# Performance work log

Hardware: AMD Instinct MI355X
Metric: run time of the kernel (lower is better)

## Reference

```python
import jax, jax.numpy as jnp
import numpy as np

B, SQ, SKV, D = 4, 2048, 2048, 2048
NEG = -1e9


def setup_inputs() -> dict:
    key = jax.random.key(0)
    ks = jax.random.split(key, 7)
    x = jax.random.normal(ks[0], (B, SKV, D), dtype=jnp.float32)
    enc_q = jax.random.normal(ks[1], (B, SQ, D), dtype=jnp.float32)
    enc_k = jax.random.normal(ks[2], (B, SKV, D), dtype=jnp.float32)
    i_mask = jax.random.bernoulli(ks[3], 0.1, (B, SQ, SKV))  # True -> masked
    s = 1.0 / np.sqrt(D)
    Wq = jax.random.normal(ks[4], (D, D), dtype=jnp.float32) * s
    Wk = jax.random.normal(ks[5], (D, D), dtype=jnp.float32) * s
    Wv = jax.random.normal(ks[6], (D, D), dtype=jnp.float32) * s
    return {"x": x, "enc_q": enc_q, "enc_k": enc_k, "i_mask": i_mask,
            "Wq": Wq, "Wk": Wk, "Wv": Wv}


def reference(x, enc_q, enc_k, i_mask, Wq, Wk, Wv):
    # Bias-free linear projections (nn.Linear: y = x @ W^T)
    q = jnp.einsum('bsd,ed->bse', enc_q, Wq)   # [B,SQ,D]
    k = jnp.einsum('bsd,ed->bse', enc_k, Wk)   # [B,SKV,D]
    v = jnp.einsum('bsd,ed->bse', x, Wv)       # [B,SKV,D]
    scale = 1.0 / jnp.sqrt(jnp.asarray(q.shape[-1], q.dtype))
    scores = jnp.einsum('bqd,bkd->bqk', q, k) * scale  # [B,SQ,SKV]
    scores = jnp.where(i_mask, jnp.asarray(NEG, scores.dtype), scores)
    attn = jax.nn.softmax(scores, axis=-1)
    return jnp.einsum('bqk,bkd->bqd', attn, v)  # [B,SQ,D]
```

## Files before the change

### kernel.cpp

```cpp
#include <hip/hip_runtime.h>
#include <stdint.h>

typedef short  short8  __attribute__((ext_vector_type(8)));
typedef unsigned short ushort8 __attribute__((ext_vector_type(8)));
typedef float  f32x4   __attribute__((ext_vector_type(4)));

#define BB  4
#define SQL 2048
#define SKL 2048
#define NEGV -1e9f
#define AS1 __attribute__((address_space(1)))
#define AS3 __attribute__((address_space(3)))

__device__ __forceinline__ unsigned short f2bf(float f){
  union { float f; uint32_t u; } x; x.f = f;
  return (unsigned short)((x.u + 0x7FFFu + ((x.u >> 16) & 1u)) >> 16);
}
__device__ __forceinline__ float bf2f(unsigned short h){
  union { uint32_t u; float f; } x; x.u = ((uint32_t)h) << 16;
  return x.f;
}

#define BARR() __builtin_amdgcn_s_barrier()
#define LGKM0() { asm volatile("s_waitcnt lgkmcnt(0)" ::: "memory"); __builtin_amdgcn_sched_barrier(0); }
#define VM0()   { asm volatile("s_waitcnt vmcnt(0)"   ::: "memory"); __builtin_amdgcn_sched_barrier(0); }

__global__ void mask_detect(const uint8_t* __restrict__ m, int* __restrict__ cnt){
  const long n4 = (long)BB * SQL * SKL / 4;
  long idx  = (long)blockIdx.x * blockDim.x + threadIdx.x;
  long step = (long)gridDim.x * blockDim.x;
  int c0 = 0, c1 = 0, c2 = 0;
  for (long i4 = idx; i4 < n4; i4 += step){
    uchar4 b = ((const uchar4*)m)[i4];
    c0 += (b.y != 0) + (b.z != 0) + (b.w != 0);
    c1 += (b.x > 1) + (b.y > 1) + (b.z > 1) + (b.w > 1);
    c2 += (b.y != 0);
  }
  #pragma unroll
  for (int o = 32; o >= 1; o >>= 1){
    c0 += __shfl_xor(c0, o); c1 += __shfl_xor(c1, o); c2 += __shfl_xor(c2, o);
  }
  if ((threadIdx.x & 63) == 0){
    atomicAdd(&cnt[0], c0); atomicAdd(&cnt[1], c1); atomicAdd(&cnt[2], c2);
  }
}

__global__ __launch_bounds__(256)
void cvt6(const float* __restrict__ s0, const float* __restrict__ s1,
          const float* __restrict__ s2, const float* __restrict__ s3,
          const float* __restrict__ s4, const float* __restrict__ s5,
          unsigned short* __restrict__ d0, unsigned short* __restrict__ d1,
          unsigned short* __restrict__ d2, unsigned short* __restrict__ d3,
          unsigned short* __restrict__ d4, unsigned short* __restrict__ d5)
{
  const long total = 7864320;
  for (long c = (long)blockIdx.x * blockDim.x + threadIdx.x; c < total;
       c += (long)gridDim.x * blockDim.x){
    const float* s; unsigned short* d; long off;
    if      (c < 2097152){ s = s0; d = d0; off = c; }
    else if (c < 4194304){ s = s1; d = d1; off = c - 2097152; }
    else if (c < 6291456){ s = s2; d = d2; off = c - 4194304; }
    else if (c < 6815744){ s = s3; d = d3; off = c - 6291456; }
    else if (c < 7340032){ s = s4; d = d4; off = c - 6815744; }
    else                 { s = s5; d = d5; off = c - 7340032; }
    f32x4 a = ((const f32x4*)s)[off * 2];
    f32x4 b = ((const f32x4*)s)[off * 2 + 1];
    ushort8 w;
    #pragma unroll
    for (int j = 0; j < 4; ++j){ w[j] = f2bf(a[j]); w[j + 4] = f2bf(b[j]); }
    ((ushort8*)d)[off] = w;
  }
}

template<int EPI>
__device__ __forceinline__ void gemm256_body(
    const unsigned short* __restrict__ Ag, const unsigned short* __restrict__ Bg,
    void* __restrict__ Cb, const void* __restrict__ mask, const int* __restrict__ cnt,
    int bz, long Cbs, long tm, long tn, float scale,
    unsigned short (&lA)[2][16384], unsigned short (&lB)[2][16384])
{
  constexpr int LD = 2048;
  const int tid = threadIdx.x, lane = tid & 63, wid = tid >> 6;
  const int wm = wid >> 2, wn = wid & 3;
  const int l15 = lane & 15, l16 = lane >> 4;

  f32x4 acc[8][4] = {};

  auto stage = [&](unsigned short* dst, const unsigned short* src, long tbase, int k){
    #pragma unroll
    for (int l = 0; l < 4; ++l){
      const int idx = l * 512 + tid;
      const int row = idx >> 3;
      const int gsw = (idx & 7) ^ (row & 7);
      __builtin_amdgcn_global_load_lds(
        (const AS1 void*)(src + (tbase + row) * LD + k + gsw * 8),
        (AS3 void*)(dst + idx * 8), 16, 0, 0);
    }
  };

  short8 aF[4], bF[4];
  #define RDA(BUF, MH, KS)                                                    \
    _Pragma("unroll")                                                         \
    for (int j = 0; j < 4; ++j){                                              \
      const int fr = wm * 128 + ((MH) * 4 + j) * 16 + l15;                    \
      const int g  = (KS) * 4 + l16;                                          \
      aF[j] = *(const short8*)&lA[BUF][(fr * 8 + (g ^ (fr & 7))) * 8];        \
    }
  #define RDB(BUF, KS)                                                        \
    _Pragma("unroll")                                                         \
    for (int j = 0; j < 4; ++j){                                              \
      const int fn = wn * 64 + j * 16 + l15;                                  \
      const int g  = (KS) * 4 + l16;                                          \
      bF[j] = *(const short8*)&lB[BUF][(fn * 8 + (g ^ (fn & 7))) * 8];        \
    }
  #define MFMA16(MH)                                                          \
    _Pragma("unroll")                                                         \
    for (int j = 0; j < 4; ++j){                                              \
      _Pragma("unroll")                                                       \
      for (int n = 0; n < 4; ++n)                                             \
        acc[(MH) * 4 + j][n] = __builtin_amdgcn_mfma_f32_16x16x32_bf16(       \
            aF[j], bF[n], acc[(MH) * 4 + j][n], 0, 0, 0);                     \
    }

  #define KTILE(BUF, KST, DOSTAGE)                                            \
  {                                                                           \
                                             \
    RDB(BUF, 0); RDA(BUF, 0, 0);                                              \
    if (DOSTAGE) stage(lA[(BUF) ^ 1], Ag, tm, (KST));                         \
    BARR(); LGKM0();                                                          \
    __builtin_amdgcn_s_setprio(1); MFMA16(0); __builtin_amdgcn_s_setprio(0);  \
    BARR();                                                                   \
                                             \
    RDA(BUF, 1, 0);                                                           \
    if (DOSTAGE) stage(lB[(BUF) ^ 1], Bg, tn, (KST));                         \
    BARR(); LGKM0();                                                          \
    __builtin_amdgcn_s_setprio(1); MFMA16(1); __builtin_amdgcn_s_setprio(0);  \
    BARR();                                                                   \
                                                            \
    RDB(BUF, 1); RDA(BUF, 0, 1);                                              \
    BARR(); LGKM0();                                                          \
    __builtin_amdgcn_s_setprio(1); MFMA16(0); __builtin_amdgcn_s_setprio(0);  \
    BARR();                                                                   \
         \
    RDA(BUF, 1, 1);                                                           \
    BARR(); LGKM0();                                                          \
    __builtin_amdgcn_s_setprio(1); MFMA16(1); __builtin_amdgcn_s_setprio(0);  \
    VM0();                                                                    \
    BARR();                                                                   \
  }

  stage(lA[0], Ag, tm, 0);
  stage(lB[0], Bg, tn, 0);
  VM0(); BARR();

  for (int it = 0; it < 16; ++it){
    KTILE(0, (2 * it + 1) * 64, true);
    KTILE(1, (2 * it + 2) * 64, it < 15);
  }

  const int colo = l15, rowg = l16 * 4;
  if constexpr (EPI == 0){
    unsigned short* C = (unsigned short*)Cb + (long)bz * Cbs;
    #pragma unroll
    for (int m = 0; m < 8; ++m)
      #pragma unroll
      for (int j = 0; j < 4; ++j){
        const long row = tm + wm * 128 + m * 16 + rowg + j;
        unsigned short* cr = C + row * LD + tn + wn * 64 + colo;
        #pragma unroll
        for (int n = 0; n < 4; ++n) cr[n * 16] = f2bf(acc[m][n][j]);
      }
  } else if constexpr (EPI == 2){
    float* C = (float*)Cb + (long)bz * Cbs;
    #pragma unroll
    for (int m = 0; m < 8; ++m)
      #pragma unroll
      for (int j = 0; j < 4; ++j){
        const long row = tm + wm * 128 + m * 16 + rowg + j;
        float* cr = C + row * LD + tn + wn * 64 + colo;
        #pragma unroll
        for (int n = 0; n < 4; ++n) cr[n * 16] = acc[m][n][j];
      }
  } else {
    const int a0 = cnt[0], a1 = cnt[1], a2 = cnt[2];
    const int mmode = (a1 == 0) ? (a0 > 1000 ? 0 : 1) : (a2 > 1000 ? 2 : 3);
    unsigned short* C = (unsigned short*)Cb + (long)bz * Cbs;
    const long mbase = (long)bz * SQL * SKL;
    #pragma unroll
    for (int m = 0; m < 8; ++m)
      #pragma unroll
      for (int j = 0; j < 4; ++j){
        const long row = tm + wm * 128 + m * 16 + rowg + j;
        #pragma unroll
        for (int n = 0; n < 4; ++n){
          const long col = tn + wn * 64 + n * 16 + colo;
          const long midx = mbase + row * SKL + col;
          bool msk;
          if (mmode == 0)      msk = ((const uint8_t*)mask)[midx] != 0;
          else if (mmode == 1) msk = ((const int*)mask)[midx] != 0;
          else if (mmode == 2) msk = ((const unsigned short*)mask)[midx] != 0;
          else                 msk = ((const uint32_t*)mask)[midx] != 0;
          float vv = acc[m][n][j] * scale;
          if (msk) vv = NEGV;
          C[row * SKL + col] = f2bf(vv);
        }
      }
  }
  #undef RDA
  #undef RDB
  #undef MFMA16
  #undef KTILE
}

__device__ __forceinline__ void xcd_decode(int& bx, int& by, int& bz){
  const int gx = gridDim.x, gy = gridDim.y;
  const int nwg = gx * gy * gridDim.z;
  const int lid = blockIdx.x + gx * (blockIdx.y + gy * blockIdx.z);
  const int sw  = (lid & 7) * (nwg >> 3) + (lid >> 3);
  bx = sw % gx;
  const int t = sw / gx;
  by = t % gy;
  bz = t / gy;
}

template<int EPI>
__global__ __launch_bounds__(512, 2)
void gemm256(const unsigned short* __restrict__ A, const unsigned short* __restrict__ B,
             void* __restrict__ Cb, const void* __restrict__ mask,
             const int* __restrict__ cnt, long Abs, long Bbs, long Cbs, float scale)
{
  __shared__ unsigned short lA[2][16384];
  __shared__ unsigned short lB[2][16384];
  int bx, by, bz; xcd_decode(bx, by, bz);
  gemm256_body<EPI>(A + (long)bz * Abs, B + (long)bz * Bbs, Cb, mask, cnt, bz, Cbs,
                    (long)by * 256, (long)bx * 256, scale, lA, lB);
}

__global__ __launch_bounds__(512, 2)
void gemm256_proj3(const unsigned short* A0, const unsigned short* A1, const unsigned short* A2,
                   const unsigned short* B0, const unsigned short* B1, const unsigned short* B2,
                   void* C0, void* C1, void* C2)
{
  __shared__ unsigned short lA[2][16384];
  __shared__ unsigned short lB[2][16384];
  int bx, by, bz; xcd_decode(bx, by, bz);
  const int sec = bz >> 2, b = bz & 3;
  const long NN = (long)SQL * 2048;
  const unsigned short* Av = sec == 0 ? A0 : sec == 1 ? A1 : A2;
  const unsigned short* Bv = sec == 0 ? B0 : sec == 1 ? B1 : B2;
  void*                 Cv = sec == 0 ? C0 : sec == 1 ? C1 : C2;
  const long Abs = (sec == 2) ? 0 : NN;
  const long Bbs = (sec == 2) ? NN : 0;
  gemm256_body<0>(Av + (long)b * Abs, Bv + (long)b * Bbs, Cv, nullptr, nullptr, b, NN,
                  (long)by * 256, (long)bx * 256, 1.f, lA, lB);
}

template<int AMODE, int BMODE, int EPI>
__device__ __forceinline__ void gemm_body(
    const void* __restrict__ Av, const void* __restrict__ Bv,
    void* __restrict__ Cb, const void* __restrict__ mask, const int* __restrict__ cnt,
    int bz, long Abs, long Bbs, long Cbs, long tm, long tn, float scale,
    unsigned short (*lA)[4096], unsigned short (*lB)[4096])
{
  constexpr int K = 2048, LD = 2048;
  const int tid = threadIdx.x, lane = tid & 63, wave = tid >> 6;
  const int wr = wave >> 1, wc = wave & 1;
  const int c0 = tid, c1 = tid + 256;
  const int r0 = c0 >> 2, q0 = (c0 & 3) * 8;
  const int r1 = c1 >> 2, q1 = (c1 & 3) * 8;

  const unsigned short* A16 = (const unsigned short*)Av + (long)bz * Abs;
  const unsigned short* B16 = (const unsigned short*)Bv + (long)bz * Bbs;
  const float*          A32 = (const float*)Av + (long)bz * Abs;
  const float*          B32 = (const float*)Bv + (long)bz * Bbs;

  f32x4 acc[4][4] = {};
  f32x4 sA[4], sB[4];

  auto issueA = [&](int buf, int kk){
    if constexpr (AMODE == 0){
      __builtin_amdgcn_global_load_lds((const AS1 void*)(A16 + (tm + r0) * LD + q0 + kk),
                                       (AS3 void*)(lA[buf] + c0 * 8), 16, 0, 0);
      __builtin_amdgcn_global_load_lds((const AS1 void*)(A16 + (tm + r1) * LD + q1 + kk),
                                       (AS3 void*)(lA[buf] + c1 * 8), 16, 0, 0);
    } else {
      sA[0] = *(const f32x4*)(A32 + (tm + r0) * LD + q0 + kk);
      sA[1] = *(const f32x4*)(A32 + (tm + r0) * LD + q0 + kk + 4);
      sA[2] = *(const f32x4*)(A32 + (tm + r1) * LD + q1 + kk);
      sA[3] = *(const f32x4*)(A32 + (tm + r1) * LD + q1 + kk + 4);
    }
  };
  auto issueB = [&](int buf, int kk){
    if constexpr (BMODE == 0){
      __builtin_amdgcn_global_load_lds((const AS1 void*)(B16 + (tn + r0) * LD + q0 + kk),
                                       (AS3 void*)(lB[buf] + c0 * 8), 16, 0, 0);
      __builtin_amdgcn_global_load_lds((const AS1 void*)(B16 + (tn + r1) * LD + q1 + kk),
                                       (AS3 void*)(lB[buf] + c1 * 8), 16, 0, 0);
    } else {
      sB[0] = *(const f32x4*)(B32 + (tn + r0) * LD + q0 + kk);
      sB[1] = *(const f32x4*)(B32 + (tn + r0) * LD + q0 + kk + 4);
      sB[2] = *(const f32x4*)(B32 + (tn + r1) * LD + q1 + kk);
      sB[3] = *(const f32x4*)(B32 + (tn + r1) * LD + q1 + kk + 4);
    }
  };
  auto writeA = [&](int buf){
    if constexpr (AMODE == 1){
      ushort8 w0, w1;
      #pragma unroll
      for (int j = 0; j < 4; ++j){
        w0[j] = f2bf(sA[0][j]); w0[j + 4] = f2bf(sA[1][j]);
        w1[j] = f2bf(sA[2][j]); w1[j + 4] = f2bf(sA[3][j]);
      }
      *(ushort8*)(lA[buf] + c0 * 8) = w0;
      *(ushort8*)(lA[buf] + c1 * 8) = w1;
    }
  };
  auto writeB = [&](int buf){
    if constexpr (BMODE == 1){
      ushort8 w0, w1;
      #pragma unroll
      for (int j = 0; j < 4; ++j){
        w0[j] = f2bf(sB[0][j]); w0[j + 4] = f2bf(sB[1][j]);
        w1[j] = f2bf(sB[2][j]); w1[j + 4] = f2bf(sB[3][j]);
      }
      *(ushort8*)(lB[buf] + c0 * 8) = w0;
      *(ushort8*)(lB[buf] + c1 * 8) = w1;
    }
  };
  auto computeTile = [&](int buf){
    short8 aF[4], bF[4];
    #pragma unroll
    for (int m = 0; m < 4; ++m)
      aF[m] = *(const short8*)(lA[buf] + (wr * 64 + m * 16 + (lane & 15)) * 32 + (lane >> 4) * 8);
    #pragma unroll
    for (int n = 0; n < 4; ++n)
      bF[n] = *(const short8*)(lB[buf] + (wc * 64 + n * 16 + (lane & 15)) * 32 + (lane >> 4) * 8);
    #pragma unroll
    for (int m = 0; m < 4; ++m)
      #pragma unroll
      for (int n = 0; n < 4; ++n)
        acc[m][n] = __builtin_amdgcn_mfma_f32_16x16x32_bf16(aF[m], bF[n], acc[m][n], 0, 0, 0);
  };

  issueA(0, 0); issueB(0, 0); writeA(0); writeB(0);
  __syncthreads();
  int cur = 0;
  for (int k0 = 0; k0 < K - 32; k0 += 32){
    issueA(cur ^ 1, k0 + 32);
    issueB(cur ^ 1, k0 + 32);
    computeTile(cur);
    writeA(cur ^ 1); writeB(cur ^ 1);
    __syncthreads();
    cur ^= 1;
  }
  computeTile(cur);

  const int colo = lane & 15, rowg = (lane >> 4) * 4;
  if constexpr (EPI == 0){
    unsigned short* C = (unsigned short*)Cb + (long)bz * Cbs;
    #pragma unroll
    for (int m = 0; m < 4; ++m)
      #pragma unroll
      for (int j = 0; j < 4; ++j){
        const long row = tm + wr * 64 + m * 16 + rowg + j;
        unsigned short* cr = C + row * LD + tn + wc * 64 + colo;
        #pragma unroll
        for (int n = 0; n < 4; ++n) cr[n * 16] = f2bf(acc[m][n][j]);
      }
  } else if constexpr (EPI == 2){
    float* C = (float*)Cb + (long)bz * Cbs;
    #pragma unroll
    for (int m = 0; m < 4; ++m)
      #pragma unroll
      for (int j = 0; j < 4; ++j){
        const long row = tm + wr * 64 + m * 16 + rowg + j;
        float* cr = C + row * LD + tn + wc * 64 + colo;
        #pragma unroll
        for (int n = 0; n < 4; ++n) cr[n * 16] = acc[m][n][j];
      }
  } else {
    const int a0 = cnt[0], a1 = cnt[1], a2 = cnt[2];
    const int mmode = (a1 == 0) ? (a0 > 1000 ? 0 : 1) : (a2 > 1000 ? 2 : 3);
    unsigned short* C = (unsigned short*)Cb + (long)bz * Cbs;
    const long mbase = (long)bz * SQL * SKL;
    #pragma unroll
    for (int m = 0; m < 4; ++m)
      #pragma unroll
      for (int j = 0; j < 4; ++j){
        const long row = tm + wr * 64 + m * 16 + rowg + j;
        #pragma unroll
        for (int n = 0; n < 4; ++n){
          const long col = tn + wc * 64 + n * 16 + colo;
          const long midx = mbase + row * SKL + col;
          bool msk;
          if (mmode == 0)      msk = ((const uint8_t*)mask)[midx] != 0;
          else if (mmode == 1) msk = ((const int*)mask)[midx] != 0;
          else if (mmode == 2) msk = ((const unsigned short*)mask)[midx] != 0;
          else                 msk = ((const uint32_t*)mask)[midx] != 0;
          float vv = acc[m][n][j] * scale;
          if (msk) vv = NEGV;
          C[row * SKL + col] = f2bf(vv);
        }
      }
  }
}

template<int AMODE, int BMODE, int EPI>
__global__ __launch_bounds__(256, 2)
void gemm_nt(const void* __restrict__ Abv, const void* __restrict__ Bbv,
             void* __restrict__ Cb, const void* __restrict__ mask,
             const int* __restrict__ cnt,
             long Abs, long Bbs, long Cbs, float scale)
{
  __shared__ unsigned short lA[2][4096];
  __shared__ unsigned short lB[2][4096];
  int bx, by, bz; xcd_decode(bx, by, bz);
  gemm_body<AMODE, BMODE, EPI>(Abv, Bbv, Cb, mask, cnt, bz, Abs, Bbs, Cbs,
                               (long)by * 128, (long)bx * 128, scale, lA, lB);
}

template<int MODE>
__global__ __launch_bounds__(256, 2)
void gemm_proj3(const void* A0, const void* A1, const void* A2,
                const void* B0, const void* B1, const void* B2,
                void* C0, void* C1, void* C2)
{
  __shared__ unsigned short lA[2][4096];
  __shared__ unsigned short lB[2][4096];
  int bx, by, bz; xcd_decode(bx, by, bz);
  const int sec = bz >> 2, b = bz & 3;
  const long NN = (long)SQL * 2048;
  const void* Av = sec == 0 ? A0 : sec == 1 ? A1 : A2;
  const void* Bv = sec == 0 ? B0 : sec == 1 ? B1 : B2;
  void*       Cv = sec == 0 ? C0 : sec == 1 ? C1 : C2;
  const long Abs = (sec == 2) ? 0 : NN;
  const long Bbs = (sec == 2) ? NN : 0;
  gemm_body<MODE, MODE, 0>(Av, Bv, Cv, nullptr, nullptr, b, Abs, Bbs, NN,
                           (long)by * 128, (long)bx * 128, 1.f, lA, lB);
}

__global__ __launch_bounds__(256, 4)
void softmax_rows(const unsigned short* __restrict__ S, unsigned short* __restrict__ P){
  const long row = blockIdx.x;
  const int t = threadIdx.x;
  ushort8 u = *((const ushort8*)(S + row * SKL) + t);
  float v[8];
  #pragma unroll
  for (int j = 0; j < 8; ++j) v[j] = bf2f(u[j]);
  float mx = v[0];
  #pragma unroll
  for (int j = 1; j < 8; ++j) mx = fmaxf(mx, v[j]);
  #pragma unroll
  for (int o = 32; o >= 1; o >>= 1) mx = fmaxf(mx, __shfl_xor(mx, o));
  __shared__ float red[8];
  const int wv = t >> 6, ln = t & 63;
  if (ln == 0) red[wv] = mx;
  __syncthreads();
  mx = fmaxf(fmaxf(red[0], red[1]), fmaxf(red[2], red[3]));
  float e[8], sum = 0.f;
  #pragma unroll
  for (int j = 0; j < 8; ++j){ e[j] = exp2f((v[j] - mx) * 1.4426950408889634f); sum += e[j]; }
  #pragma unroll
  for (int o = 32; o >= 1; o >>= 1) sum += __shfl_xor(sum, o);
  if (ln == 0) red[4 + wv] = sum;
  __syncthreads();
  sum = red[4] + red[5] + red[6] + red[7];
  const float inv = 1.0f / sum;
  ushort8 o8;
  #pragma unroll
  for (int j = 0; j < 8; ++j) o8[j] = f2bf(e[j] * inv);
  *((ushort8*)(P + row * SKL) + t) = o8;
}

extern "C" void kernel_launch(void* const* d_in, const int* in_sizes, int n_in,
                              void* d_out, int out_size, void* d_ws, size_t ws_size,
                              hipStream_t stream)
{
  (void)in_sizes; (void)n_in; (void)out_size;
  const void* x    = d_in[0];
  const void* encq = d_in[1];
  const void* enck = d_in[2];
  const void* imsk = d_in[3];
  const void* Wq   = d_in[4];
  const void* Wk   = d_in[5];
  const void* Wv   = d_in[6];

  uint8_t* ws = (uint8_t*)d_ws;
  int* cnt = (int*)ws;
  const long NN = (long)2048 * 2048;
  const float scale = 0.022097086912079608f;

  hipMemsetAsync(cnt, 0, 4096, stream);
  mask_detect<<<256, 256, 0, stream>>>((const uint8_t*)imsk, cnt);

  const size_t ENC = 33554432, WSZ = 8388608;
  const size_t FULL_NEED = 4096 + 3 * ENC + 3 * WSZ + 2 * ENC;
  if (ws_size >= FULL_NEED){
    unsigned short* xb  = (unsigned short*)(ws + 4096);
    unsigned short* qb  = xb + 16777216;
    unsigned short* kb  = qb + 16777216;
    unsigned short* Wqb = kb + 16777216;
    unsigned short* Wkb = Wqb + 4194304;
    unsigned short* Wvb = Wkb + 4194304;
    unsigned short* Kp  = Wvb + 4194304;
    unsigned short* Vt  = Kp + 16777216;
    unsigned short* Q   = (unsigned short*)d_out;
    unsigned short* S   = Q + 16777216;
    unsigned short* P   = qb;

    cvt6<<<2048, 256, 0, stream>>>((const float*)x, (const float*)encq, (const float*)enck,
                                   (const float*)Wq, (const float*)Wk, (const float*)Wv,
                                   xb, qb, kb, Wqb, Wkb, Wvb);
    gemm256_proj3<<<dim3(8, 8, 12), 512, 0, stream>>>(qb, kb, Wvb, Wqb, Wkb, xb, Q, Kp, Vt);
    gemm256<1><<<dim3(8, 8, BB), 512, 0, stream>>>(Q, Kp, S, imsk, cnt, NN, NN, NN, scale);
    softmax_rows<<<BB * SQL, 256, 0, stream>>>(S, P);
    gemm256<2><<<dim3(8, 8, BB), 512, 0, stream>>>(P, Vt, d_out, nullptr, cnt, NN, NN, NN, 1.f);
  } else {
    unsigned short* Q  = (unsigned short*)(ws + 4096);
    unsigned short* Kp = Q  + 16777216;
    unsigned short* Vt = Kp + 16777216;
    unsigned short* P  = Q;
    unsigned short* S;
    const size_t need = 4096 + 4ull * 33554432;
    if (ws_size >= need) S = Vt + 16777216;
    else                 S = (unsigned short*)d_out;

    gemm_proj3<1><<<dim3(16, 16, 12), 256, 0, stream>>>(encq, enck, Wv, Wq, Wk, x, Q, Kp, Vt);
    gemm_nt<0, 0, 1><<<dim3(16, 16, BB), 256, 0, stream>>>(Q, Kp, S, imsk, cnt, NN, NN, NN, scale);
    softmax_rows<<<BB * SQL, 256, 0, stream>>>(S, P);
    gemm_nt<0, 0, 2><<<dim3(16, 16, BB), 256, 0, stream>>>(P, Vt, d_out, nullptr, cnt, NN, NN, NN, 1.f);
  }
}
```

Measured before the change: 543.4 us.

## Restructure GEMM mainloop into quadrant-based 8-wave ping-pong with finer load staging

Reorganizes the 256x256 GEMM tile so each wave computes four 64x32 quadrants, staging A and B halves separately into the next LDS buffer between quadrant MFMA groups. Partial vmcnt waits replace full drains, aiming to overlap global-to-LDS loads with MFMA work and shorten per-tile stalls. The last K tile gets a separate no-prefetch path. This changes the register layout of accumulators and fragments and relies on the async staging count being correct for the partial waits.

```diff
diff --git a/kernel.cpp b/kernel.cpp
--- a/kernel.cpp
+++ b/kernel.cpp
@@ -23,7 +23,9 @@
 
 #define BARR() __builtin_amdgcn_s_barrier()
 #define LGKM0() { asm volatile("s_waitcnt lgkmcnt(0)" ::: "memory"); __builtin_amdgcn_sched_barrier(0); }
-#define VM0()   { asm volatile("s_waitcnt vmcnt(0)"   ::: "memory"); __builtin_amdgcn_sched_barrier(0); }
+#define VMW(N)  { asm volatile("s_waitcnt vmcnt(" #N ")" ::: "memory"); __builtin_amdgcn_sched_barrier(0); }
+#define PRIO1 __builtin_amdgcn_s_setprio(1)
+#define PRIO0 __builtin_amdgcn_s_setprio(0)
 
 __global__ void mask_detect(const uint8_t* __restrict__ m, int* __restrict__ cnt){
   const long n4 = (long)BB * SQL * SKL / 4;
@@ -84,132 +86,173 @@
   const int wm = wid >> 2, wn = wid & 3;
   const int l15 = lane & 15, l16 = lane >> 4;
 
-  f32x4 acc[8][4] = {};
-
-  auto stage = [&](unsigned short* dst, const unsigned short* src, long tbase, int k){
-    #pragma unroll
-    for (int l = 0; l < 4; ++l){
+  f32x4 acc[2][2][4][2] = {};
+  short8 aF[4][2];
+  short8 bF[2][2][2];
+
+  auto stageA = [&](int buf, int half, int k){
+    const unsigned short* s = Ag + (tm + half * 128) * LD + k;
+    unsigned short* d = lA[buf] + half * 8192;
+    #pragma unroll
+    for (int l = 0; l < 2; ++l){
       const int idx = l * 512 + tid;
-      const int row = idx >> 3;
-      const int gsw = (idx & 7) ^ (row & 7);
-      __builtin_amdgcn_global_load_lds(
-        (const AS1 void*)(src + (tbase + row) * LD + k + gsw * 8),
-        (AS3 void*)(dst + idx * 8), 16, 0, 0);
+      const int r   = idx >> 3;
+      const int gsw = (idx & 7) ^ (r & 7);
+      __builtin_amdgcn_global_load_lds((const AS1 void*)(s + r * LD + gsw * 8),
+                                       (AS3 void*)(d + idx * 8), 16, 0, 0);
     }
   };
-
-  short8 aF[4], bF[4];
-  #define RDA(BUF, MH, KS)                                                    \
+  auto stageB = [&](int buf, int half, int k){
+    const unsigned short* s = Bg + (tn + half * 128) * LD + k;
+    unsigned short* d = lB[buf] + half * 8192;
+    #pragma unroll
+    for (int l = 0; l < 2; ++l){
+      const int idx = l * 512 + tid;
+      const int r   = idx >> 3;
+      const int gsw = (idx & 7) ^ (r & 7);
+      __builtin_amdgcn_global_load_lds((const AS1 void*)(s + r * LD + gsw * 8),
+                                       (AS3 void*)(d + idx * 8), 16, 0, 0);
+    }
+  };
+
+  #define RD_A(BUF, QM)                                                       \
     _Pragma("unroll")                                                         \
-    for (int j = 0; j < 4; ++j){                                              \
-      const int fr = wm * 128 + ((MH) * 4 + j) * 16 + l15;                    \
-      const int g  = (KS) * 4 + l16;                                          \
-      aF[j] = *(const short8*)&lA[BUF][(fr * 8 + (g ^ (fr & 7))) * 8];        \
-    }
-  #define RDB(BUF, KS)                                                        \
+    for (int mr = 0; mr < 4; ++mr)                                            \
+      _Pragma("unroll")                                                       \
+      for (int ks = 0; ks < 2; ++ks){                                         \
+        const int r = (QM) * 128 + wm * 64 + mr * 16 + l15;                   \
+        const int g = ks * 4 + l16;                                           \
+        aF[mr][ks] = *(const short8*)&lA[BUF][(r * 8 + (g ^ (r & 7))) * 8];   \
+      }
+  #define RD_B(BUF, QN)                                                       \
     _Pragma("unroll")                                                         \
-    for (int j = 0; j < 4; ++j){                                              \
-      const int fn = wn * 64 + j * 16 + l15;                                  \
-      const int g  = (KS) * 4 + l16;                                          \
-      bF[j] = *(const short8*)&lB[BUF][(fn * 8 + (g ^ (fn & 7))) * 8];        \
-    }
-  #define MFMA16(MH)                                                          \
+    for (int nr = 0; nr < 2; ++nr)                                            \
+      _Pragma("unroll")                                                       \
+      for (int ks = 0; ks < 2; ++ks){                                         \
+        const int c = (QN) * 128 + wn * 32 + nr * 16 + l15;                   \
+        const int g = ks * 4 + l16;                                           \
+        bF[QN][nr][ks] = *(const short8*)&lB[BUF][(c * 8 + (g ^ (c & 7))) * 8]; \
+      }
+  #define MFMA16(QM, QN)                                                      \
     _Pragma("unroll")                                                         \
-    for (int j = 0; j < 4; ++j){                                              \
+    for (int mr = 0; mr < 4; ++mr)                                            \
       _Pragma("unroll")                                                       \
-      for (int n = 0; n < 4; ++n)                                             \
-        acc[(MH) * 4 + j][n] = __builtin_amdgcn_mfma_f32_16x16x32_bf16(       \
-            aF[j], bF[n], acc[(MH) * 4 + j][n], 0, 0, 0);                     \
-    }
-
-  #define KTILE(BUF, KST, DOSTAGE)                                            \
+      for (int nr = 0; nr < 2; ++nr)                                          \
+        _Pragma("unroll")                                                     \
+        for (int ks = 0; ks < 2; ++ks)                                        \
+          acc[QM][QN][mr][nr] = __builtin_amdgcn_mfma_f32_16x16x32_bf16(      \
+              aF[mr][ks], bF[QN][nr][ks], acc[QM][QN][mr][nr], 0, 0, 0);
+
+  #define KTILE_MAIN(BUF, KNXT)                                               \
   {                                                                           \
-                                             \
-    RDB(BUF, 0); RDA(BUF, 0, 0);                                              \
-    if (DOSTAGE) stage(lA[(BUF) ^ 1], Ag, tm, (KST));                         \
+    RD_A(BUF, 0); RD_B(BUF, 0);                                               \
+    stageA((BUF) ^ 1, 0, (KNXT));                                             \
     BARR(); LGKM0();                                                          \
-    __builtin_amdgcn_s_setprio(1); MFMA16(0); __builtin_amdgcn_s_setprio(0);  \
+    PRIO1; MFMA16(0, 0); PRIO0; VMW(4); BARR();                               \
+    RD_B(BUF, 1);                                                             \
+    stageB((BUF) ^ 1, 0, (KNXT));                                             \
+    BARR(); LGKM0();                                                          \
+    PRIO1; MFMA16(0, 1); PRIO0; VMW(4); BARR();                               \
+    RD_A(BUF, 1);                                                             \
+    stageB((BUF) ^ 1, 1, (KNXT));                                             \
+    BARR(); LGKM0();                                                          \
+    PRIO1; MFMA16(1, 1); PRIO0; BARR();                                       \
+    stageA((BUF) ^ 1, 1, (KNXT));                                             \
     BARR();                                                                   \
-                                             \
-    RDA(BUF, 1, 0);                                                           \
-    if (DOSTAGE) stage(lB[(BUF) ^ 1], Bg, tn, (KST));                         \
+    PRIO1; MFMA16(1, 0); PRIO0; VMW(4); BARR();                               \
+  }
+  #define KTILE_LAST(BUF)                                                     \
+  {                                                                           \
+    RD_A(BUF, 0); RD_B(BUF, 0);                                               \
     BARR(); LGKM0();                                                          \
-    __builtin_amdgcn_s_setprio(1); MFMA16(1); __builtin_amdgcn_s_setprio(0);  \
-    BARR();                                                                   \
-                                                            \
-    RDB(BUF, 1); RDA(BUF, 0, 1);                                              \
+    PRIO1; MFMA16(0, 0); PRIO0; VMW(2); BARR();                               \
+    RD_B(BUF, 1);                                                             \
     BARR(); LGKM0();                                                          \
-    __builtin_amdgcn_s_setprio(1); MFMA16(0); __builtin_amdgcn_s_setprio(0);  \
-    BARR();                                                                   \
-         \
-    RDA(BUF, 1, 1);                                                           \
+    PRIO1; MFMA16(0, 1); PRIO0; VMW(0); BARR();                               \
+    RD_A(BUF, 1);                                                             \
     BARR(); LGKM0();                                                          \
-    __builtin_amdgcn_s_setprio(1); MFMA16(1); __builtin_amdgcn_s_setprio(0);  \
-    VM0();                                                                    \
-    BARR();                                                                   \
-  }
-
-  stage(lA[0], Ag, tm, 0);
-  stage(lB[0], Bg, tn, 0);
-  VM0(); BARR();
-
-  for (int it = 0; it < 16; ++it){
-    KTILE(0, (2 * it + 1) * 64, true);
-    KTILE(1, (2 * it + 2) * 64, it < 15);
-  }
+    PRIO1; MFMA16(1, 1); PRIO0; BARR();                                       \
+    PRIO1; MFMA16(1, 0); PRIO0;                                               \
+  }
+
+  stageA(0, 0, 0);
+  stageB(0, 0, 0);
+  stageB(0, 1, 0);
+  stageA(0, 1, 0);
+  VMW(4); BARR();
+
+  for (int it = 0; it < 15; ++it){
+    KTILE_MAIN(0, (2 * it + 1) * 64);
+    KTILE_MAIN(1, (2 * it + 2) * 64);
+  }
+  KTILE_MAIN(0, 31 * 64);
+  KTILE_LAST(1);
 
   const int colo = l15, rowg = l16 * 4;
   if constexpr (EPI == 0){
     unsigned short* C = (unsigned short*)Cb + (long)bz * Cbs;
     #pragma unroll
-    for (int m = 0; m < 8; ++m)
-      #pragma unroll
-      for (int j = 0; j < 4; ++j){
-        const long row = tm + wm * 128 + m * 16 + rowg + j;
-        unsigned short* cr = C + row * LD + tn + wn * 64 + colo;
+    for (int qm = 0; qm < 2; ++qm)
+      #pragma unroll
+      for (int qn = 0; qn < 2; ++qn)
         #pragma unroll
-        for (int n = 0; n < 4; ++n) cr[n * 16] = f2bf(acc[m][n][j]);
-      }
+        for (int mr = 0; mr < 4; ++mr)
+          #pragma unroll
+          for (int j = 0; j < 4; ++j){
+            const long row = tm + qm * 128 + wm * 64 + mr * 16 + rowg + j;
+            unsigned short* cr = C + row * LD + tn + qn * 128 + wn * 32 + colo;
+            #pragma unroll
+            for (int nr = 0; nr < 2; ++nr) cr[nr * 16] = f2bf(acc[qm][qn][mr][nr][j]);
+          }
   } else if constexpr (EPI == 2){
     float* C = (float*)Cb + (long)bz * Cbs;
     #pragma unroll
-    for (int m = 0; m < 8; ++m)
-      #pragma unroll
-      for (int j = 0; j < 4; ++j){
-        const long row = tm + wm * 128 + m * 16 + rowg + j;
-        float* cr = C + row * LD + tn + wn * 64 + colo;
+    for (int qm = 0; qm < 2; ++qm)
+      #pragma unroll
+      for (int qn = 0; qn < 2; ++qn)
         #pragma unroll
-        for (int n = 0; n < 4; ++n) cr[n * 16] = acc[m][n][j];
-      }
+        for (int mr = 0; mr < 4; ++mr)
+          #pragma unroll
+          for (int j = 0; j < 4; ++j){
+            const long row = tm + qm * 128 + wm * 64 + mr * 16 + rowg + j;
+            float* cr = C + row * LD + tn + qn * 128 + wn * 32 + colo;
+            #pragma unroll
+            for (int nr = 0; nr < 2; ++nr) cr[nr * 16] = acc[qm][qn][mr][nr][j];
+          }
   } else {
     const int a0 = cnt[0], a1 = cnt[1], a2 = cnt[2];
     const int mmode = (a1 == 0) ? (a0 > 1000 ? 0 : 1) : (a2 > 1000 ? 2 : 3);
     unsigned short* C = (unsigned short*)Cb + (long)bz * Cbs;
     const long mbase = (long)bz * SQL * SKL;
     #pragma unroll
-    for (int m = 0; m < 8; ++m)
-      #pragma unroll
-      for (int j = 0; j < 4; ++j){
-        const long row = tm + wm * 128 + m * 16 + rowg + j;
+    for (int qm = 0; qm < 2; ++qm)
+      #pragma unroll
+      for (int qn = 0; qn < 2; ++qn)
         #pragma unroll
-        for (int n = 0; n < 4; ++n){
-          const long col = tn + wn * 64 + n * 16 + colo;
-          const long midx = mbase + row * SKL + col;
-          bool msk;
-          if (mmode == 0)      msk = ((const uint8_t*)mask)[midx] != 0;
-          else if (mmode == 1) msk = ((const int*)mask)[midx] != 0;
-          else if (mmode == 2) msk = ((const unsigned short*)mask)[midx] != 0;
-          else                 msk = ((const uint32_t*)mask)[midx] != 0;
-          float vv = acc[m][n][j] * scale;
-          if (msk) vv = NEGV;
-          C[row * SKL + col] = f2bf(vv);
-        }
-      }
-  }
-  #undef RDA
-  #undef RDB
+        for (int mr = 0; mr < 4; ++mr)
+          #pragma unroll
+          for (int j = 0; j < 4; ++j){
+            const long row = tm + qm * 128 + wm * 64 + mr * 16 + rowg + j;
+            #pragma unroll
+            for (int nr = 0; nr < 2; ++nr){
+              const long col = tn + qn * 128 + wn * 32 + nr * 16 + colo;
+              const long midx = mbase + row * SKL + col;
+              bool msk;
+              if (mmode == 0)      msk = ((const uint8_t*)mask)[midx] != 0;
+              else if (mmode == 1) msk = ((const int*)mask)[midx] != 0;
+              else if (mmode == 2) msk = ((const unsigned short*)mask)[midx] != 0;
+              else                 msk = ((const uint32_t*)mask)[midx] != 0;
+              float vv = acc[qm][qn][mr][nr][j] * scale;
+              if (msk) vv = NEGV;
+              C[row * SKL + col] = f2bf(vv);
+            }
+          }
+  }
+  #undef RD_A
+  #undef RD_B
   #undef MFMA16
-  #undef KTILE
+  #undef KTILE_MAIN
+  #undef KTILE_LAST
 }
 
 __device__ __forceinline__ void xcd_decode(int& bx, int& by, int& bz){
```

New measurement: 523.9 us. 3.6% less time.

## Restructure 256x256 GEMM into 4-wave, 4-stage K=32 pipelined mainloop

Applied to the files above, without the earlier changes.

Rewrites the main bf16 GEMM body from 8 waves with a 2-stage K=64 double buffer to 4 waves, each computing a 128x128 sub-tile (8x8 MFMA accumulators). It uses a 4-deep K=32 LDS ring with partial vmcnt/lgkmcnt waits and register double-buffered fragments. The aim is to overlap global-to-LDS loads, LDS reads and MFMAs with one barrier per K step and fewer LDS reads per MFMA. In exchange, register pressure rises sharply (256 accumulator floats plus 32 fragment registers) and occupancy drops to one 256-thread block per launch bound, which risks spills or less latency hiding.

```diff
diff --git a/kernel.cpp b/kernel.cpp
--- a/kernel.cpp
+++ b/kernel.cpp
@@ -21,9 +21,9 @@
   return x.f;
 }
 
-#define BARR() __builtin_amdgcn_s_barrier()
-#define LGKM0() { asm volatile("s_waitcnt lgkmcnt(0)" ::: "memory"); __builtin_amdgcn_sched_barrier(0); }
-#define VM0()   { asm volatile("s_waitcnt vmcnt(0)"   ::: "memory"); __builtin_amdgcn_sched_barrier(0); }
+#define SBAR() { __builtin_amdgcn_s_barrier(); __builtin_amdgcn_sched_barrier(0); }
+#define LGKMW(N) { asm volatile("s_waitcnt lgkmcnt(" #N ")" ::: "memory"); __builtin_amdgcn_sched_barrier(0); }
+#define VMW(N)   { asm volatile("s_waitcnt vmcnt(" #N ")"   ::: "memory"); __builtin_amdgcn_sched_barrier(0); }
 
 __global__ void mask_detect(const uint8_t* __restrict__ m, int* __restrict__ cnt){
   const long n4 = (long)BB * SQL * SKL / 4;
@@ -77,109 +77,90 @@
     const unsigned short* __restrict__ Ag, const unsigned short* __restrict__ Bg,
     void* __restrict__ Cb, const void* __restrict__ mask, const int* __restrict__ cnt,
     int bz, long Cbs, long tm, long tn, float scale,
-    unsigned short (&lA)[2][16384], unsigned short (&lB)[2][16384])
+    unsigned short (&lA)[4][8192], unsigned short (&lB)[4][8192])
 {
   constexpr int LD = 2048;
   const int tid = threadIdx.x, lane = tid & 63, wid = tid >> 6;
-  const int wm = wid >> 2, wn = wid & 3;
+  const int wm = wid >> 1, wn = wid & 1;
   const int l15 = lane & 15, l16 = lane >> 4;
 
-  f32x4 acc[8][4] = {};
-
-  auto stage = [&](unsigned short* dst, const unsigned short* src, long tbase, int k){
+  f32x4 acc[8][8] = {};
+  short8 aF0[8], bF0[8], aF1[8], bF1[8];
+
+  const int g8    = (l16 ^ (l15 & 3)) * 8;
+  const int offA0 = (wm * 128 + l15) * 32 + g8;
+  const int offB0 = (wn * 128 + l15) * 32 + g8;
+
+  auto stage = [&](int buf, int kt){
     #pragma unroll
     for (int l = 0; l < 4; ++l){
-      const int idx = l * 512 + tid;
-      const int row = idx >> 3;
-      const int gsw = (idx & 7) ^ (row & 7);
+      const int idx = l * 256 + tid;
+      const int row = idx >> 2;
+      const int gsw = ((idx & 3) ^ (row & 3)) * 8;
       __builtin_amdgcn_global_load_lds(
-        (const AS1 void*)(src + (tbase + row) * LD + k + gsw * 8),
-        (AS3 void*)(dst + idx * 8), 16, 0, 0);
+        (const AS1 void*)(Ag + (tm + row) * LD + kt * 32 + gsw),
+        (AS3 void*)(lA[buf] + idx * 8), 16, 0, 0);
+      __builtin_amdgcn_global_load_lds(
+        (const AS1 void*)(Bg + (tn + row) * LD + kt * 32 + gsw),
+        (AS3 void*)(lB[buf] + idx * 8), 16, 0, 0);
     }
   };
 
-  short8 aF[4], bF[4];
-  #define RDA(BUF, MH, KS)                                                    \
+  #define RDF(PX, BUF) {                                                      \
     _Pragma("unroll")                                                         \
-    for (int j = 0; j < 4; ++j){                                              \
-      const int fr = wm * 128 + ((MH) * 4 + j) * 16 + l15;                    \
-      const int g  = (KS) * 4 + l16;                                          \
-      aF[j] = *(const short8*)&lA[BUF][(fr * 8 + (g ^ (fr & 7))) * 8];        \
-    }
-  #define RDB(BUF, KS)                                                        \
+    for (int mr = 0; mr < 8; ++mr)                                            \
+      aF##PX[mr] = *(const short8*)&lA[(BUF)][offA0 + mr * 512];              \
     _Pragma("unroll")                                                         \
-    for (int j = 0; j < 4; ++j){                                              \
-      const int fn = wn * 64 + j * 16 + l15;                                  \
-      const int g  = (KS) * 4 + l16;                                          \
-      bF[j] = *(const short8*)&lB[BUF][(fn * 8 + (g ^ (fn & 7))) * 8];        \
-    }
-  #define MFMA16(MH)                                                          \
+    for (int nr = 0; nr < 8; ++nr)                                            \
+      bF##PX[nr] = *(const short8*)&lB[(BUF)][offB0 + nr * 512];              \
+  }
+  #define MM(PX) {                                                            \
     _Pragma("unroll")                                                         \
-    for (int j = 0; j < 4; ++j){                                              \
+    for (int mr = 0; mr < 8; ++mr)                                            \
       _Pragma("unroll")                                                       \
-      for (int n = 0; n < 4; ++n)                                             \
-        acc[(MH) * 4 + j][n] = __builtin_amdgcn_mfma_f32_16x16x32_bf16(       \
-            aF[j], bF[n], acc[(MH) * 4 + j][n], 0, 0, 0);                     \
-    }
-
-  #define KTILE(BUF, KST, DOSTAGE)                                            \
-  {                                                                           \
-                                             \
-    RDB(BUF, 0); RDA(BUF, 0, 0);                                              \
-    if (DOSTAGE) stage(lA[(BUF) ^ 1], Ag, tm, (KST));                         \
-    BARR(); LGKM0();                                                          \
-    __builtin_amdgcn_s_setprio(1); MFMA16(0); __builtin_amdgcn_s_setprio(0);  \
-    BARR();                                                                   \
-                                             \
-    RDA(BUF, 1, 0);                                                           \
-    if (DOSTAGE) stage(lB[(BUF) ^ 1], Bg, tn, (KST));                         \
-    BARR(); LGKM0();                                                          \
-    __builtin_amdgcn_s_setprio(1); MFMA16(1); __builtin_amdgcn_s_setprio(0);  \
-    BARR();                                                                   \
-                                                            \
-    RDB(BUF, 1); RDA(BUF, 0, 1);                                              \
-    BARR(); LGKM0();                                                          \
-    __builtin_amdgcn_s_setprio(1); MFMA16(0); __builtin_amdgcn_s_setprio(0);  \
-    BARR();                                                                   \
-         \
-    RDA(BUF, 1, 1);                                                           \
-    BARR(); LGKM0();                                                          \
-    __builtin_amdgcn_s_setprio(1); MFMA16(1); __builtin_amdgcn_s_setprio(0);  \
-    VM0();                                                                    \
-    BARR();                                                                   \
-  }
-
-  stage(lA[0], Ag, tm, 0);
-  stage(lB[0], Bg, tn, 0);
-  VM0(); BARR();
-
-  for (int it = 0; it < 16; ++it){
-    KTILE(0, (2 * it + 1) * 64, true);
-    KTILE(1, (2 * it + 2) * 64, it < 15);
-  }
+      for (int nr = 0; nr < 8; ++nr)                                          \
+        acc[mr][nr] = __builtin_amdgcn_mfma_f32_16x16x32_bf16(                \
+            aF##PX[mr], bF##PX[nr], acc[mr][nr], 0, 0, 0);                    \
+  }
+
+  stage(0, 0); stage(1, 1); stage(2, 2);
+  VMW(8); SBAR();
+  RDF(0, 0);
+
+  for (int it = 0; it < 15; ++it){
+    const int kt = it * 4;
+    RDF(1, 1); LGKMW(15); MM(0); stage(3, kt + 3); VMW(8); SBAR();
+    RDF(0, 2); LGKMW(15); MM(1); stage(0, kt + 4); VMW(8); SBAR();
+    RDF(1, 3); LGKMW(15); MM(0); stage(1, kt + 5); VMW(8); SBAR();
+    RDF(0, 0); LGKMW(15); MM(1); stage(2, kt + 6); VMW(8); SBAR();
+  }
+  RDF(1, 1); LGKMW(15); MM(0); stage(3, 63); VMW(8); SBAR();
+  RDF(0, 2); LGKMW(15); MM(1); VMW(0); SBAR();
+  RDF(1, 3); LGKMW(15); MM(0); SBAR();
+  LGKMW(0); MM(1);
 
   const int colo = l15, rowg = l16 * 4;
   if constexpr (EPI == 0){
     unsigned short* C = (unsigned short*)Cb + (long)bz * Cbs;
     #pragma unroll
-    for (int m = 0; m < 8; ++m)
-      #pragma unroll
-      for (int j = 0; j < 4; ++j){
-        const long row = tm + wm * 128 + m * 16 + rowg + j;
-        unsigned short* cr = C + row * LD + tn + wn * 64 + colo;
+    for (int mr = 0; mr < 8; ++mr)
+      #pragma unroll
+      for (int j = 0; j < 4; ++j){
+        const long row = tm + wm * 128 + mr * 16 + rowg + j;
+        unsigned short* cr = C + row * LD + tn + wn * 128 + colo;
         #pragma unroll
-        for (int n = 0; n < 4; ++n) cr[n * 16] = f2bf(acc[m][n][j]);
+        for (int nr = 0; nr < 8; ++nr) cr[nr * 16] = f2bf(acc[mr][nr][j]);
       }
   } else if constexpr (EPI == 2){
     float* C = (float*)Cb + (long)bz * Cbs;
     #pragma unroll
-    for (int m = 0; m < 8; ++m)
-      #pragma unroll
-      for (int j = 0; j < 4; ++j){
-        const long row = tm + wm * 128 + m * 16 + rowg + j;
-        float* cr = C + row * LD + tn + wn * 64 + colo;
+    for (int mr = 0; mr < 8; ++mr)
+      #pragma unroll
+      for (int j = 0; j < 4; ++j){
+        const long row = tm + wm * 128 + mr * 16 + rowg + j;
+        float* cr = C + row * LD + tn + wn * 128 + colo;
         #pragma unroll
-        for (int n = 0; n < 4; ++n) cr[n * 16] = acc[m][n][j];
+        for (int nr = 0; nr < 8; ++nr) cr[nr * 16] = acc[mr][nr][j];
       }
   } else {
     const int a0 = cnt[0], a1 = cnt[1], a2 = cnt[2];
@@ -187,29 +168,27 @@
     unsigned short* C = (unsigned short*)Cb + (long)bz * Cbs;
     const long mbase = (long)bz * SQL * SKL;
     #pragma unroll
-    for (int m = 0; m < 8; ++m)
-      #pragma unroll
-      for (int j = 0; j < 4; ++j){
-        const long row = tm + wm * 128 + m * 16 + rowg + j;
+    for (int mr = 0; mr < 8; ++mr)
+      #pragma unroll
+      for (int j = 0; j < 4; ++j){
+        const long row = tm + wm * 128 + mr * 16 + rowg + j;
         #pragma unroll
-        for (int n = 0; n < 4; ++n){
-          const long col = tn + wn * 64 + n * 16 + colo;
+        for (int nr = 0; nr < 8; ++nr){
+          const long col = tn + wn * 128 + nr * 16 + colo;
           const long midx = mbase + row * SKL + col;
           bool msk;
           if (mmode == 0)      msk = ((const uint8_t*)mask)[midx] != 0;
           else if (mmode == 1) msk = ((const int*)mask)[midx] != 0;
           else if (mmode == 2) msk = ((const unsigned short*)mask)[midx] != 0;
           else                 msk = ((const uint32_t*)mask)[midx] != 0;
-          float vv = acc[m][n][j] * scale;
+          float vv = acc[mr][nr][j] * scale;
           if (msk) vv = NEGV;
           C[row * SKL + col] = f2bf(vv);
         }
       }
   }
-  #undef RDA
-  #undef RDB
-  #undef MFMA16
-  #undef KTILE
+  #undef RDF
+  #undef MM
 }
 
 __device__ __forceinline__ void xcd_decode(int& bx, int& by, int& bz){
@@ -224,25 +203,25 @@
 }
 
 template<int EPI>
-__global__ __launch_bounds__(512, 2)
+__global__ __launch_bounds__(256, 1)
 void gemm256(const unsigned short* __restrict__ A, const unsigned short* __restrict__ B,
              void* __restrict__ Cb, const void* __restrict__ mask,
              const int* __restrict__ cnt, long Abs, long Bbs, long Cbs, float scale)
 {
-  __shared__ unsigned short lA[2][16384];
-  __shared__ unsigned short lB[2][16384];
+  __shared__ unsigned short lA[4][8192];
+  __shared__ unsigned short lB[4][8192];
   int bx, by, bz; xcd_decode(bx, by, bz);
   gemm256_body<EPI>(A + (long)bz * Abs, B + (long)bz * Bbs, Cb, mask, cnt, bz, Cbs,
                     (long)by * 256, (long)bx * 256, scale, lA, lB);
 }
 
-__global__ __launch_bounds__(512, 2)
+__global__ __launch_bounds__(256, 1)
 void gemm256_proj3(const unsigned short* A0, const unsigned short* A1, const unsigned short* A2,
                    const unsigned short* B0, const unsigned short* B1, const unsigned short* B2,
                    void* C0, void* C1, void* C2)
 {
-  __shared__ unsigned short lA[2][16384];
-  __shared__ unsigned short lB[2][16384];
+  __shared__ unsigned short lA[4][8192];
+  __shared__ unsigned short lB[4][8192];
   int bx, by, bz; xcd_decode(bx, by, bz);
   const int sec = bz >> 2, b = bz & 3;
   const long NN = (long)SQL * 2048;
@@ -511,10 +490,10 @@
     cvt6<<<2048, 256, 0, stream>>>((const float*)x, (const float*)encq, (const float*)enck,
                                    (const float*)Wq, (const float*)Wk, (const float*)Wv,
                                    xb, qb, kb, Wqb, Wkb, Wvb);
-    gemm256_proj3<<<dim3(8, 8, 12), 512, 0, stream>>>(qb, kb, Wvb, Wqb, Wkb, xb, Q, Kp, Vt);
-    gemm256<1><<<dim3(8, 8, BB), 512, 0, stream>>>(Q, Kp, S, imsk, cnt, NN, NN, NN, scale);
+    gemm256_proj3<<<dim3(8, 8, 12), 256, 0, stream>>>(qb, kb, Wvb, Wqb, Wkb, xb, Q, Kp, Vt);
+    gemm256<1><<<dim3(8, 8, BB), 256, 0, stream>>>(Q, Kp, S, imsk, cnt, NN, NN, NN, scale);
     softmax_rows<<<BB * SQL, 256, 0, stream>>>(S, P);
-    gemm256<2><<<dim3(8, 8, BB), 512, 0, stream>>>(P, Vt, d_out, nullptr, cnt, NN, NN, NN, 1.f);
+    gemm256<2><<<dim3(8, 8, BB), 256, 0, stream>>>(P, Vt, d_out, nullptr, cnt, NN, NN, NN, 1.f);
   } else {
     unsigned short* Q  = (unsigned short*)(ws + 4096);
     unsigned short* Kp = Q  + 16777216;
```

Result: slower. 707.7 us (+30.2%).
